# Optimization experiments

Measured on AMD Instinct MI355X. Metric: run time of the kernel, lower is better.

## Reference

```python
import jax, jax.numpy as jnp
import numpy as np

B, T, D, E, P = 4, 2048, 1024, 8, 1024

def setup_inputs() -> dict:
    key = jax.random.key(0)
    k1, k2, k3 = jax.random.split(key, 3)
    x = jax.random.normal(k1, (B, T, D), dtype=jnp.float32)
    gate_w = jax.random.normal(k2, (D, E), dtype=jnp.float32) * (1.0 / np.sqrt(D))
    gate_b = jnp.zeros((E,), dtype=jnp.float32)
    expert_w = jax.random.normal(k3, (E, D, P), dtype=jnp.float32) * (1.0 / np.sqrt(D))
    expert_b = jnp.zeros((E, P), dtype=jnp.float32)
    return {"x": x, "gate_w": gate_w, "gate_b": gate_b,
            "expert_w": expert_w, "expert_b": expert_b}

def reference(x, gate_w, gate_b, expert_w, expert_b):
    # gating: Dense(E) with softmax -> [B, T, E]
    gate = jax.nn.softmax(jnp.einsum('btd,de->bte', x, gate_w) + gate_b, axis=-1)
    # all experts as one batched GEMM: [B, T, E, P]
    expert_out = jnp.einsum('btd,edp->btep', x, expert_w) + expert_b
    # gate-weighted sum over experts -> [B, T, P]
    out = jnp.einsum('bte,btep->btp', gate, expert_out)
    return out
```

## Files before the change

kernel.cpp:

```cpp
#include <hip/hip_runtime.h>
#include <hip/hip_bf16.h>
#include <math.h>

#define M_TOT 8192
#define D_DIM 1024
#define E_NUM 8
#define P_DIM 1024
#define K_TOT (E_NUM * D_DIM)

typedef __attribute__((ext_vector_type(8))) short short8;
typedef __attribute__((ext_vector_type(4))) float f32x4;
typedef __attribute__((ext_vector_type(8))) unsigned short u16x8;

static __device__ __forceinline__ unsigned short f2bf(float f) {
  unsigned u = __builtin_bit_cast(unsigned, f);
  unsigned r = (u + 0x7fffu + ((u >> 16) & 1u)) >> 16;
  return (unsigned short)r;
}

__global__ __launch_bounds__(256) void gate_kernel(const float* __restrict__ x,
                                                   const float* __restrict__ gw,
                                                   const float* __restrict__ gb,
                                                   float* __restrict__ gate) {
  const int row  = blockIdx.x * 4 + (threadIdx.x >> 6);
  const int lane = threadIdx.x & 63;
  const float* xr = x + (size_t)row * D_DIM;
  float acc[E_NUM];
#pragma unroll
  for (int e = 0; e < E_NUM; ++e) acc[e] = 0.f;
#pragma unroll
  for (int it = 0; it < 16; ++it) {
    const int d = it * 64 + lane;
    const float xv = xr[d];
    const float4* g4 = reinterpret_cast<const float4*>(gw + (size_t)d * E_NUM);
    float4 a = g4[0], b = g4[1];
    acc[0] += xv * a.x; acc[1] += xv * a.y; acc[2] += xv * a.z; acc[3] += xv * a.w;
    acc[4] += xv * b.x; acc[5] += xv * b.y; acc[6] += xv * b.z; acc[7] += xv * b.w;
  }
#pragma unroll
  for (int off = 32; off >= 1; off >>= 1) {
#pragma unroll
    for (int e = 0; e < E_NUM; ++e) acc[e] += __shfl_xor(acc[e], off, 64);
  }
  if (lane == 0) {
    float v[E_NUM], mx = -1e30f;
#pragma unroll
    for (int e = 0; e < E_NUM; ++e) { v[e] = acc[e] + gb[e]; mx = fmaxf(mx, v[e]); }
    float s = 0.f;
#pragma unroll
    for (int e = 0; e < E_NUM; ++e) { v[e] = expf(v[e] - mx); s += v[e]; }
    const float inv = 1.f / s;
#pragma unroll
    for (int e = 0; e < E_NUM; ++e) gate[(size_t)row * E_NUM + e] = v[e] * inv;
  }
}

__global__ __launch_bounds__(256) void wtrans2_kernel(const float* __restrict__ w,
                                                      unsigned short* __restrict__ wt) {
  __shared__ float tile[64][65];
  const int e  = blockIdx.z;
  const int p0 = blockIdx.y * 64;
  const int d0 = blockIdx.x * 64;
  const int tx = threadIdx.x & 63;
  const int ty = threadIdx.x >> 6;
  const float* src = w + ((size_t)e * D_DIM + d0) * P_DIM + p0;
#pragma unroll
  for (int i = 0; i < 16; ++i) {
    const int dr = i * 4 + ty;
    tile[dr][tx] = src[(size_t)dr * P_DIM + tx];
  }
  __syncthreads();
#pragma unroll
  for (int i = 0; i < 16; ++i) {
    const int pr = i * 4 + ty;
    const int c = tx ^ ((pr & 7) << 3);
    wt[(size_t)(p0 + pr) * K_TOT + e * D_DIM + d0 + c] = f2bf(tile[tx][pr]);
  }
}

__global__ __launch_bounds__(256) void xb_kernel(const float* __restrict__ x,
                                                 unsigned short* __restrict__ xb) {
  const int tid = threadIdx.x;
  const int m   = blockIdx.x * 2 + (tid >> 7);
  const int jd  = tid & 127;
  const float4* xp = reinterpret_cast<const float4*>(x + (size_t)m * D_DIM + jd * 8);
  const float4 p = xp[0], q = xp[1];
  const int cbase = (jd >> 3) * 8 + ((jd & 7) ^ (m & 7));
  u16x8 v;
  v[0] = f2bf(p.x); v[1] = f2bf(p.y); v[2] = f2bf(p.z); v[3] = f2bf(p.w);
  v[4] = f2bf(q.x); v[5] = f2bf(q.y); v[6] = f2bf(q.z); v[7] = f2bf(q.w);
  *reinterpret_cast<u16x8*>(&xb[(size_t)m * D_DIM + cbase * 8]) = v;
}

__global__ __launch_bounds__(256, 4) void gemm_ex_kernel(
    const unsigned short* __restrict__ xb,
    const unsigned short* __restrict__ wt,
    const float* __restrict__ gate,
    const float* __restrict__ eb,
    float* __restrict__ out) {
  __shared__ unsigned short lA[128 * 64];
  __shared__ unsigned short lB[128 * 64];
  __shared__ float lG[128 * 8];

  const int tid  = threadIdx.x;
  const int lane = tid & 63;
  const int wid  = tid >> 6;
  const int wr   = wid >> 1, wc = wid & 1;

  const int bid = blockIdx.x;
  const int nt  = bid & 7;
  const int idx = bid >> 3;
  const int kh  = idx & 1;
  const int mt  = idx >> 1;
  const int m0  = mt * 128, n0 = nt * 128;

  reinterpret_cast<float4*>(lG)[tid] =
      reinterpret_cast<const float4*>(gate + (size_t)m0 * E_NUM)[tid];

  f32x4 acc[4][4];
#pragma unroll
  for (int i = 0; i < 4; ++i)
#pragma unroll
    for (int j = 0; j < 4; ++j)
#pragma unroll
      for (int k = 0; k < 4; ++k) acc[i][j][k] = 0.f;

  const int r0 = tid >> 3;
  const int c8 = tid & 7;
  const unsigned short* pAb = xb + (size_t)(m0 + r0) * D_DIM + c8 * 8;
  const unsigned short* pBb = wt + (size_t)(n0 + r0) * K_TOT + c8 * 8;

  for (int e = 0; e < 4; ++e) {
    const int eg = kh * 4 + e;
    if (e > 0) {
#pragma unroll
      for (int m = 0; m < 4; ++m) {
#pragma unroll
        for (int reg = 0; reg < 4; ++reg) {
          const int r = wr * 64 + m * 16 + (lane >> 4) * 4 + reg;
          const float ratio = lG[r * 8 + (eg - 1)] / lG[r * 8 + eg];
#pragma unroll
          for (int n = 0; n < 4; ++n) acc[m][n][reg] *= ratio;
        }
      }
    }
    const unsigned short* pB = pBb + (size_t)eg * D_DIM;
    for (int kt = 0; kt < 16; ++kt) {
      __syncthreads();
#pragma unroll
      for (int i = 0; i < 4; ++i) {
        __builtin_amdgcn_global_load_lds(
            (const __attribute__((address_space(1))) void*)(pAb + (size_t)i * 32 * D_DIM + kt * 64),
            (__attribute__((address_space(3))) void*)&lA[(tid + i * 256) * 8], 16, 0, 0);
      }
#pragma unroll
      for (int i = 0; i < 4; ++i) {
        __builtin_amdgcn_global_load_lds(
            (const __attribute__((address_space(1))) void*)(pB + (size_t)i * 32 * K_TOT + kt * 64),
            (__attribute__((address_space(3))) void*)&lB[(tid + i * 256) * 8], 16, 0, 0);
      }
      __syncthreads();
#pragma unroll
      for (int kk = 0; kk < 2; ++kk) {
        const int e0 = kk * 32 + (lane >> 4) * 8;
        short8 a[4], b[4];
#pragma unroll
        for (int m = 0; m < 4; ++m) {
          const int r = wr * 64 + m * 16 + (lane & 15);
          a[m] = *reinterpret_cast<const short8*>(&lA[r * 64 + (e0 ^ ((r & 7) << 3))]);
        }
#pragma unroll
        for (int n = 0; n < 4; ++n) {
          const int r = wc * 64 + n * 16 + (lane & 15);
          b[n] = *reinterpret_cast<const short8*>(&lB[r * 64 + (e0 ^ ((r & 7) << 3))]);
        }
#pragma unroll
        for (int m = 0; m < 4; ++m)
#pragma unroll
          for (int n = 0; n < 4; ++n)
            acc[m][n] = __builtin_amdgcn_mfma_f32_16x16x32_bf16(a[m], b[n], acc[m][n], 0, 0, 0);
      }
    }
  }

#pragma unroll
  for (int n = 0; n < 4; ++n) {
    const int cl = wc * 64 + n * 16 + (lane & 15);
    float lb[E_NUM];
    if (kh == 0) {
#pragma unroll
      for (int e = 0; e < E_NUM; ++e) lb[e] = eb[(size_t)e * P_DIM + n0 + cl];
    }
#pragma unroll
    for (int m = 0; m < 4; ++m) {
#pragma unroll
      for (int reg = 0; reg < 4; ++reg) {
        const int r  = wr * 64 + m * 16 + (lane >> 4) * 4 + reg;
        const float gl = lG[r * 8 + kh * 4 + 3];
        float v = acc[m][n][reg] * gl;
        if (kh == 0) {
          float bsum = 0.f;
#pragma unroll
          for (int e = 0; e < E_NUM; ++e) bsum += lG[r * 8 + e] * lb[e];
          v += bsum;
        }
        atomicAdd(&out[(size_t)(m0 + r) * P_DIM + n0 + cl], v);
      }
    }
  }
}


__global__ __launch_bounds__(256) void wtrans_kernel(const float* __restrict__ w,
                                                     unsigned short* __restrict__ wt) {
  __shared__ float tile[64][65];
  const int e  = blockIdx.z;
  const int p0 = blockIdx.y * 64;
  const int d0 = blockIdx.x * 64;
  const int tx = threadIdx.x & 63;
  const int ty = threadIdx.x >> 6;
  const float* src = w + ((size_t)e * D_DIM + d0) * P_DIM + p0;
#pragma unroll
  for (int i = 0; i < 16; ++i) {
    const int dr = i * 4 + ty;
    tile[dr][tx] = src[(size_t)dr * P_DIM + tx];
  }
  __syncthreads();
  unsigned short* dst = wt + ((size_t)e * P_DIM + p0) * D_DIM + d0;
#pragma unroll
  for (int i = 0; i < 16; ++i) {
    const int pr = i * 4 + ty;
    const int cc = tx ^ ((pr & 7) << 3);
    dst[(size_t)pr * D_DIM + cc] = f2bf(tile[tx][pr]);
  }
}

__global__ __launch_bounds__(256, 2) void moe_gemm_kernel(
    const float* __restrict__ x,
    const unsigned short* __restrict__ wt,
    const float* __restrict__ gate,
    const float* __restrict__ eb,
    float* __restrict__ out) {
  __shared__ unsigned short lA[128 * 64];
  __shared__ unsigned short lB[128 * 64];
  __shared__ float lG[128 * 8];
  __shared__ float lBias[E_NUM * 128];

  const int tid  = threadIdx.x;
  const int lane = tid & 63;
  const int wid  = tid >> 6;
  const int wr   = wid >> 1, wc = wid & 1;
  const int m0   = blockIdx.x * 128;
  const int n0   = blockIdx.y * 128;

  reinterpret_cast<float4*>(lG)[tid] =
      reinterpret_cast<const float4*>(gate + (size_t)m0 * E_NUM)[tid];
  {
    const int e = tid >> 5, cc = (tid & 31) * 4;
    *reinterpret_cast<float4*>(&lBias[e * 128 + cc]) =
        *reinterpret_cast<const float4*>(&eb[(size_t)e * P_DIM + n0 + cc]);
  }
  __syncthreads();

  const int rA   = tid >> 1;
  const int colA = (tid & 1) * 32;
  const float* xrow = x + (size_t)(m0 + rA) * D_DIM + colA;

  f32x4 acc[4][4];
#pragma unroll
  for (int i = 0; i < 4; ++i)
#pragma unroll
    for (int jj = 0; jj < 4; ++jj)
#pragma unroll
      for (int k = 0; k < 4; ++k) acc[i][jj][k] = 0.f;

  for (int e = 0; e < E_NUM; ++e) {
    const float gs = lG[rA * 8 + e];
    const unsigned short* wte = wt + ((size_t)e * P_DIM + n0) * D_DIM;
    for (int kt = 0; kt < 16; ++kt) {
      __syncthreads();
      const float4* apv = reinterpret_cast<const float4*>(xrow + kt * 64);
#pragma unroll
      for (int jj = 0; jj < 4; ++jj) {
        float4 p = apv[2 * jj], q = apv[2 * jj + 1];
        u16x8 v;
        v[0] = f2bf(p.x * gs); v[1] = f2bf(p.y * gs);
        v[2] = f2bf(p.z * gs); v[3] = f2bf(p.w * gs);
        v[4] = f2bf(q.x * gs); v[5] = f2bf(q.y * gs);
        v[6] = f2bf(q.z * gs); v[7] = f2bf(q.w * gs);
        const int idx = rA * 64 + ((colA + jj * 8) ^ ((rA & 7) << 3));
        *reinterpret_cast<u16x8*>(&lA[idx]) = v;
      }
#pragma unroll
      for (int i = 0; i < 4; ++i) {
        const int u  = tid + i * 256;
        const int rr = u >> 3;
        const int cc = u & 7;
        const unsigned short* src = wte + (size_t)rr * D_DIM + kt * 64 + cc * 8;
        __builtin_amdgcn_global_load_lds(
            (const __attribute__((address_space(1))) void*)src,
            (__attribute__((address_space(3))) void*)&lB[u * 8], 16, 0, 0);
      }
      __syncthreads();
#pragma unroll
      for (int kk = 0; kk < 2; ++kk) {
        const int e0 = kk * 32 + (lane >> 4) * 8;
        short8 a[4], b[4];
#pragma unroll
        for (int m = 0; m < 4; ++m) {
          const int r = wr * 64 + m * 16 + (lane & 15);
          a[m] = *reinterpret_cast<const short8*>(&lA[r * 64 + (e0 ^ ((r & 7) << 3))]);
        }
#pragma unroll
        for (int n = 0; n < 4; ++n) {
          const int r = wc * 64 + n * 16 + (lane & 15);
          b[n] = *reinterpret_cast<const short8*>(&lB[r * 64 + (e0 ^ ((r & 7) << 3))]);
        }
#pragma unroll
        for (int m = 0; m < 4; ++m)
#pragma unroll
          for (int n = 0; n < 4; ++n)
            acc[m][n] = __builtin_amdgcn_mfma_f32_16x16x32_bf16(a[m], b[n], acc[m][n], 0, 0, 0);
      }
    }
  }

#pragma unroll
  for (int m = 0; m < 4; ++m) {
#pragma unroll
    for (int n = 0; n < 4; ++n) {
      const int rbase = wr * 64 + m * 16 + ((lane >> 4) * 4);
      const int cl    = wc * 64 + n * 16 + (lane & 15);
#pragma unroll
      for (int reg = 0; reg < 4; ++reg) {
        const int r = rbase + reg;
        float bsum = 0.f;
#pragma unroll
        for (int e = 0; e < E_NUM; ++e) bsum += lG[r * 8 + e] * lBias[e * 128 + cl];
        out[(size_t)(m0 + r) * P_DIM + n0 + cl] = acc[m][n][reg] + bsum;
      }
    }
  }
}


extern "C" void kernel_launch(void* const* d_in, const int* in_sizes, int n_in,
                              void* d_out, int out_size, void* d_ws, size_t ws_size,
                              hipStream_t stream) {
  const float* x  = (const float*)d_in[0];
  const float* gw = (const float*)d_in[1];
  const float* gb = (const float*)d_in[2];
  const float* ew = (const float*)d_in[3];
  const float* eb = (const float*)d_in[4];
  float* out = (float*)d_out;

  char* ws = (char*)d_ws;
  float* gate        = (float*)ws;
  unsigned short* wt = (unsigned short*)(ws + 262144);

  const size_t need_new = 262144ull + 16777216ull + 16777216ull;

  gate_kernel<<<M_TOT / 4, 256, 0, stream>>>(x, gw, gb, gate);

  if (ws_size >= need_new) {
    unsigned short* xbb = (unsigned short*)(ws + 262144 + 16777216);
    hipMemsetAsync(d_out, 0, (size_t)out_size * sizeof(float), stream);
    wtrans2_kernel<<<dim3(D_DIM / 64, P_DIM / 64, E_NUM), 256, 0, stream>>>(ew, wt);
    xb_kernel<<<M_TOT / 2, 256, 0, stream>>>(x, xbb);
    gemm_ex_kernel<<<1024, 256, 0, stream>>>(xbb, wt, gate, eb, out);
  } else {
    wtrans_kernel<<<dim3(D_DIM / 64, P_DIM / 64, E_NUM), 256, 0, stream>>>(ew, wt);
    moe_gemm_kernel<<<dim3(M_TOT / 128, P_DIM / 128), 256, 0, stream>>>(x, wt, gate, eb, out);
  }
}
```

Measured before the change: 190.1 us.

## Fuse gate with bf16 x cast, split-K over four expert pairs, bias-init output

The gating kernel now also converts x to swizzled bf16, which removes the separate xb pass and one read of x. The memset and the bias epilogue are replaced by a kernel that writes gate-weighted bias sums into out. The GEMM now splits K four ways (two experts per block, 2048 blocks) instead of two, which raises parallelism but doubles the atomic traffic into out. Gate values are read from global memory rather than LDS, and occupancy is hinted at 5 blocks per SM.

```diff
diff --git a/kernel.cpp b/kernel.cpp
--- a/kernel.cpp
+++ b/kernel.cpp
@@ -18,22 +18,29 @@
   return (unsigned short)r;
 }
 
-__global__ __launch_bounds__(256) void gate_kernel(const float* __restrict__ x,
-                                                   const float* __restrict__ gw,
-                                                   const float* __restrict__ gb,
-                                                   float* __restrict__ gate) {
+__global__ __launch_bounds__(256) void gate_xb_kernel(const float* __restrict__ x,
+                                                      const float* __restrict__ gw,
+                                                      const float* __restrict__ gb,
+                                                      float* __restrict__ gate,
+                                                      unsigned short* __restrict__ xb) {
   const int row  = blockIdx.x * 4 + (threadIdx.x >> 6);
   const int lane = threadIdx.x & 63;
-  const float* xr = x + (size_t)row * D_DIM;
+  const float* xr = x + (size_t)row * D_DIM + lane * 16;
+  float xx[16];
+#pragma unroll
+  for (int q = 0; q < 4; ++q) {
+    const float4 v = reinterpret_cast<const float4*>(xr)[q];
+    xx[q * 4 + 0] = v.x; xx[q * 4 + 1] = v.y; xx[q * 4 + 2] = v.z; xx[q * 4 + 3] = v.w;
+  }
   float acc[E_NUM];
 #pragma unroll
   for (int e = 0; e < E_NUM; ++e) acc[e] = 0.f;
 #pragma unroll
-  for (int it = 0; it < 16; ++it) {
-    const int d = it * 64 + lane;
-    const float xv = xr[d];
+  for (int j = 0; j < 16; ++j) {
+    const int d = lane * 16 + j;
     const float4* g4 = reinterpret_cast<const float4*>(gw + (size_t)d * E_NUM);
-    float4 a = g4[0], b = g4[1];
+    const float4 a = g4[0], b = g4[1];
+    const float xv = xx[j];
     acc[0] += xv * a.x; acc[1] += xv * a.y; acc[2] += xv * a.z; acc[3] += xv * a.w;
     acc[4] += xv * b.x; acc[5] += xv * b.y; acc[6] += xv * b.z; acc[7] += xv * b.w;
   }
@@ -52,6 +59,16 @@
     const float inv = 1.f / s;
 #pragma unroll
     for (int e = 0; e < E_NUM; ++e) gate[(size_t)row * E_NUM + e] = v[e] * inv;
+  }
+  unsigned short* xrow = xb + (size_t)row * D_DIM;
+#pragma unroll
+  for (int h = 0; h < 2; ++h) {
+    const int jd = lane * 2 + h;
+    const int cbase = (jd >> 3) * 8 + ((jd & 7) ^ (row & 7));
+    u16x8 v;
+#pragma unroll
+    for (int k = 0; k < 8; ++k) v[k] = f2bf(xx[h * 8 + k]);
+    *reinterpret_cast<u16x8*>(&xrow[cbase * 8]) = v;
   }
 }
 
@@ -78,29 +95,29 @@
   }
 }
 
-__global__ __launch_bounds__(256) void xb_kernel(const float* __restrict__ x,
-                                                 unsigned short* __restrict__ xb) {
-  const int tid = threadIdx.x;
-  const int m   = blockIdx.x * 2 + (tid >> 7);
-  const int jd  = tid & 127;
-  const float4* xp = reinterpret_cast<const float4*>(x + (size_t)m * D_DIM + jd * 8);
-  const float4 p = xp[0], q = xp[1];
-  const int cbase = (jd >> 3) * 8 + ((jd & 7) ^ (m & 7));
-  u16x8 v;
-  v[0] = f2bf(p.x); v[1] = f2bf(p.y); v[2] = f2bf(p.z); v[3] = f2bf(p.w);
-  v[4] = f2bf(q.x); v[5] = f2bf(q.y); v[6] = f2bf(q.z); v[7] = f2bf(q.w);
-  *reinterpret_cast<u16x8*>(&xb[(size_t)m * D_DIM + cbase * 8]) = v;
-}
-
-__global__ __launch_bounds__(256, 4) void gemm_ex_kernel(
+__global__ __launch_bounds__(256) void biasinit_kernel(const float* __restrict__ gate,
+                                                       const float* __restrict__ eb,
+                                                       float* __restrict__ out) {
+  const int m = blockIdx.x;
+  const int p = threadIdx.x * 4;
+  const float* g = gate + (size_t)m * E_NUM;
+  float4 s = {0.f, 0.f, 0.f, 0.f};
+#pragma unroll
+  for (int e = 0; e < E_NUM; ++e) {
+    const float ge = g[e];
+    const float4 b4 = *reinterpret_cast<const float4*>(&eb[(size_t)e * P_DIM + p]);
+    s.x += ge * b4.x; s.y += ge * b4.y; s.z += ge * b4.z; s.w += ge * b4.w;
+  }
+  *reinterpret_cast<float4*>(&out[(size_t)m * P_DIM + p]) = s;
+}
+
+__global__ __launch_bounds__(256, 5) void gemm_sk4_kernel(
     const unsigned short* __restrict__ xb,
     const unsigned short* __restrict__ wt,
     const float* __restrict__ gate,
-    const float* __restrict__ eb,
     float* __restrict__ out) {
   __shared__ unsigned short lA[128 * 64];
   __shared__ unsigned short lB[128 * 64];
-  __shared__ float lG[128 * 8];
 
   const int tid  = threadIdx.x;
   const int lane = tid & 63;
@@ -110,12 +127,10 @@
   const int bid = blockIdx.x;
   const int nt  = bid & 7;
   const int idx = bid >> 3;
-  const int kh  = idx & 1;
-  const int mt  = idx >> 1;
+  const int kq  = idx & 3;
+  const int mt  = idx >> 2;
   const int m0  = mt * 128, n0 = nt * 128;
-
-  reinterpret_cast<float4*>(lG)[tid] =
-      reinterpret_cast<const float4*>(gate + (size_t)m0 * E_NUM)[tid];
+  const int e0x = kq * 2;
 
   f32x4 acc[4][4];
 #pragma unroll
@@ -128,23 +143,26 @@
   const int r0 = tid >> 3;
   const int c8 = tid & 7;
   const unsigned short* pAb = xb + (size_t)(m0 + r0) * D_DIM + c8 * 8;
-  const unsigned short* pBb = wt + (size_t)(n0 + r0) * K_TOT + c8 * 8;
-
-  for (int e = 0; e < 4; ++e) {
-    const int eg = kh * 4 + e;
-    if (e > 0) {
+  const unsigned short* pBb = wt + (size_t)(n0 + r0) * K_TOT + (size_t)e0x * D_DIM + c8 * 8;
+
+  float gl[16];
+
+  for (int e = 0; e < 2; ++e) {
+    if (e == 1) {
 #pragma unroll
       for (int m = 0; m < 4; ++m) {
 #pragma unroll
         for (int reg = 0; reg < 4; ++reg) {
           const int r = wr * 64 + m * 16 + (lane >> 4) * 4 + reg;
-          const float ratio = lG[r * 8 + (eg - 1)] / lG[r * 8 + eg];
+          const float2 gp = *reinterpret_cast<const float2*>(&gate[(size_t)(m0 + r) * E_NUM + e0x]);
+          gl[m * 4 + reg] = gp.y;
+          const float ratio = gp.x / gp.y;
 #pragma unroll
           for (int n = 0; n < 4; ++n) acc[m][n][reg] *= ratio;
         }
       }
     }
-    const unsigned short* pB = pBb + (size_t)eg * D_DIM;
+    const unsigned short* pB = pBb + (size_t)e * D_DIM;
     for (int kt = 0; kt < 16; ++kt) {
       __syncthreads();
 #pragma unroll
@@ -186,30 +204,54 @@
 #pragma unroll
   for (int n = 0; n < 4; ++n) {
     const int cl = wc * 64 + n * 16 + (lane & 15);
-    float lb[E_NUM];
-    if (kh == 0) {
-#pragma unroll
-      for (int e = 0; e < E_NUM; ++e) lb[e] = eb[(size_t)e * P_DIM + n0 + cl];
+#pragma unroll
+    for (int m = 0; m < 4; ++m) {
+#pragma unroll
+      for (int reg = 0; reg < 4; ++reg) {
+        const int r = wr * 64 + m * 16 + (lane >> 4) * 4 + reg;
+        atomicAdd(&out[(size_t)(m0 + r) * P_DIM + n0 + cl], acc[m][n][reg] * gl[m * 4 + reg]);
+      }
     }
-#pragma unroll
-    for (int m = 0; m < 4; ++m) {
-#pragma unroll
-      for (int reg = 0; reg < 4; ++reg) {
-        const int r  = wr * 64 + m * 16 + (lane >> 4) * 4 + reg;
-        const float gl = lG[r * 8 + kh * 4 + 3];
-        float v = acc[m][n][reg] * gl;
-        if (kh == 0) {
-          float bsum = 0.f;
-#pragma unroll
-          for (int e = 0; e < E_NUM; ++e) bsum += lG[r * 8 + e] * lb[e];
-          v += bsum;
-        }
-        atomicAdd(&out[(size_t)(m0 + r) * P_DIM + n0 + cl], v);
-      }
-    }
-  }
-}
-
+  }
+}
+
+
+__global__ __launch_bounds__(256) void gate_kernel(const float* __restrict__ x,
+                                                   const float* __restrict__ gw,
+                                                   const float* __restrict__ gb,
+                                                   float* __restrict__ gate) {
+  const int row  = blockIdx.x * 4 + (threadIdx.x >> 6);
+  const int lane = threadIdx.x & 63;
+  const float* xr = x + (size_t)row * D_DIM;
+  float acc[E_NUM];
+#pragma unroll
+  for (int e = 0; e < E_NUM; ++e) acc[e] = 0.f;
+#pragma unroll
+  for (int it = 0; it < 16; ++it) {
+    const int d = it * 64 + lane;
+    const float xv = xr[d];
+    const float4* g4 = reinterpret_cast<const float4*>(gw + (size_t)d * E_NUM);
+    float4 a = g4[0], b = g4[1];
+    acc[0] += xv * a.x; acc[1] += xv * a.y; acc[2] += xv * a.z; acc[3] += xv * a.w;
+    acc[4] += xv * b.x; acc[5] += xv * b.y; acc[6] += xv * b.z; acc[7] += xv * b.w;
+  }
+#pragma unroll
+  for (int off = 32; off >= 1; off >>= 1) {
+#pragma unroll
+    for (int e = 0; e < E_NUM; ++e) acc[e] += __shfl_xor(acc[e], off, 64);
+  }
+  if (lane == 0) {
+    float v[E_NUM], mx = -1e30f;
+#pragma unroll
+    for (int e = 0; e < E_NUM; ++e) { v[e] = acc[e] + gb[e]; mx = fmaxf(mx, v[e]); }
+    float s = 0.f;
+#pragma unroll
+    for (int e = 0; e < E_NUM; ++e) { v[e] = expf(v[e] - mx); s += v[e]; }
+    const float inv = 1.f / s;
+#pragma unroll
+    for (int e = 0; e < E_NUM; ++e) gate[(size_t)row * E_NUM + e] = v[e] * inv;
+  }
+}
 
 __global__ __launch_bounds__(256) void wtrans_kernel(const float* __restrict__ w,
                                                      unsigned short* __restrict__ wt) {
@@ -360,15 +402,14 @@
 
   const size_t need_new = 262144ull + 16777216ull + 16777216ull;
 
-  gate_kernel<<<M_TOT / 4, 256, 0, stream>>>(x, gw, gb, gate);
-
   if (ws_size >= need_new) {
     unsigned short* xbb = (unsigned short*)(ws + 262144 + 16777216);
-    hipMemsetAsync(d_out, 0, (size_t)out_size * sizeof(float), stream);
+    gate_xb_kernel<<<M_TOT / 4, 256, 0, stream>>>(x, gw, gb, gate, xbb);
     wtrans2_kernel<<<dim3(D_DIM / 64, P_DIM / 64, E_NUM), 256, 0, stream>>>(ew, wt);
-    xb_kernel<<<M_TOT / 2, 256, 0, stream>>>(x, xbb);
-    gemm_ex_kernel<<<1024, 256, 0, stream>>>(xbb, wt, gate, eb, out);
+    biasinit_kernel<<<M_TOT, 256, 0, stream>>>(gate, eb, out);
+    gemm_sk4_kernel<<<2048, 256, 0, stream>>>(xbb, wt, gate, out);
   } else {
+    gate_kernel<<<M_TOT / 4, 256, 0, stream>>>(x, gw, gb, gate);
     wtrans_kernel<<<dim3(D_DIM / 64, P_DIM / 64, E_NUM), 256, 0, stream>>>(ew, wt);
     moe_gemm_kernel<<<dim3(M_TOT / 128, P_DIM / 128), 256, 0, stream>>>(x, wt, gate, eb, out);
   }
```

Result: slower. 266.7 us (+40.3%).
